# Kernel optimization log

Measured on AMD Instinct MI355X. Metric: run time of the kernel, lower is better.

Reference implementation:

```python
import jax, jax.numpy as jnp
import numpy as np

N_GRAPHS = 100
BN_EPS = 1e-5
L = 4


def batch_norm(x, gamma, beta):
    # torch BatchNorm1d in training mode: biased batch statistics over the node dim
    mu = jnp.mean(x, axis=0)
    var = jnp.var(x, axis=0)
    return gamma * (x - mu) * jax.lax.rsqrt(var + BN_EPS) + beta


def setup_inputs() -> dict:
    key = jax.random.key(0)
    ks = jax.random.split(key, 24)
    N, E, IN, H, C = 50000, 600000, 128, 128, 10
    s = 0.05
    inp = {
        "h": jax.random.normal(ks[0], (N, IN), jnp.float32),
        "snorm_n": jax.random.uniform(ks[1], (N, 1), jnp.float32),
        "edge_src": jax.random.randint(ks[2], (E,), 0, N, jnp.int32),
        "edge_dst": jax.random.randint(ks[3], (E,), 0, N, jnp.int32),
        "graph_ids": jnp.sort(jax.random.randint(ks[4], (N,), 0, N_GRAPHS, jnp.int32)),
        # embedding_h
        "emb_W": jax.random.normal(ks[5], (IN, H), jnp.float32) * s,
        "emb_b": jnp.zeros((H,), jnp.float32),
        # per-layer GIN params, stacked over L layers
        "eps": jnp.zeros((L,), jnp.float32),
        "W1": jax.random.normal(ks[6], (L, H, H), jnp.float32) * s,
        "b1": jnp.zeros((L, H), jnp.float32),
        "g1": jnp.ones((L, H), jnp.float32),   # MLP internal BN gamma
        "be1": jnp.zeros((L, H), jnp.float32),  # MLP internal BN beta
        "W2": jax.random.normal(ks[7], (L, H, H), jnp.float32) * s,
        "b2": jnp.zeros((L, H), jnp.float32),
        "ga": jnp.ones((L, H), jnp.float32),    # ApplyNodeFunc BN gamma
        "ba": jnp.zeros((L, H), jnp.float32),
        "gl": jnp.ones((L, H), jnp.float32),    # GINLayer node BN gamma
        "bl": jnp.zeros((L, H), jnp.float32),
        # linears_prediction (L+1 of them)
        "pred_W": jax.random.normal(ks[8], (L + 1, H, C), jnp.float32) * s,
        "pred_b": jnp.zeros((L + 1, C), jnp.float32),
    }
    return inp


def reference(h, snorm_n, edge_src, edge_dst, graph_ids, emb_W, emb_b, eps,
              W1, b1, g1, be1, W2, b2, ga, ba, gl, bl, pred_W, pred_b):
    N = h.shape[0]
    h = h @ emb_W + emb_b  # embedding_h
    hidden_rep = [h]
    for i in range(L):
        h_in = h
        # sum-aggregate neighbor features (irregular gather + scatter-add)
        neigh = jax.ops.segment_sum(h[edge_src], edge_dst, num_segments=N)
        z = (1.0 + eps[i]) * h + neigh
        # ApplyNodeFunc: MLP (lin->BN->relu->lin) then BN then relu
        z = jax.nn.relu(batch_norm(z @ W1[i] + b1[i], g1[i], be1[i]))
        z = z @ W2[i] + b2[i]
        z = jax.nn.relu(batch_norm(z, ga[i], ba[i]))
        z = z * snorm_n                      # graph_norm
        z = batch_norm(z, gl[i], bl[i])      # batch_norm
        z = jax.nn.relu(z)
        h = h_in + z                         # residual (dropout p=0)
        hidden_rep.append(h)
    score = jnp.zeros((N_GRAPHS, pred_W.shape[-1]), h.dtype)
    for i, hr in enumerate(hidden_rep):
        pooled = jax.ops.segment_sum(hr, graph_ids, num_segments=N_GRAPHS)
        score = score + pooled @ pred_W[i] + pred_b[i]
    return score
```

## Files before the change

kernel.cpp:

```cpp
#include <hip/hip_runtime.h>

#define HD __device__ __forceinline__

static constexpr int H = 128;
static constexpr int G = 100;
static constexpr int L = 4;
static constexpr int C = 10;
static constexpr int DEGCAP = 64;

typedef __attribute__((ext_vector_type(8))) short short8;
typedef __attribute__((ext_vector_type(4))) float f32x4;

HD float bf2f(unsigned int u16) {
    return __uint_as_float(u16 << 16);
}
HD unsigned int f2bf(float f) {
    unsigned int u = __float_as_uint(f);
    u += 0x7fffu + ((u >> 16) & 1u);
    return u >> 16;
}

__global__ __launch_bounds__(256) void prep_kernel(
    const float* __restrict__ embW, const float* __restrict__ W1, const float* __restrict__ W2,
    unsigned short* __restrict__ WT, unsigned short* __restrict__ Hb,
    const int* __restrict__ src, const int* __restrict__ dst, int E,
    int* __restrict__ cnt, int* __restrict__ esrc) {
    int b = blockIdx.x;
    if (b < 576) {
        int mat = b >> 6;
        int bx = b & 63;
        if (b == 0 && threadIdx.x < 64)
            ((unsigned int*)Hb)[threadIdx.x] = 0u;
        const float* s = (mat == 0) ? embW
                       : (mat <= L) ? W1 + (size_t)(mat - 1) * H * H
                                    : W2 + (size_t)(mat - 1 - L) * H * H;
        int t = bx * 256 + threadIdx.x;
        int col = t >> 7, k = t & 127;
        WT[(size_t)mat * H * H + col * H + k] = (unsigned short)f2bf(s[(size_t)k * H + col]);
    } else {
        int e = (b - 576) * 256 + threadIdx.x;
        if (e < E) {
            int d = dst[e];
            int pos = atomicAdd(&cnt[d], 1) & (DEGCAP - 1);
            esrc[(size_t)d * DEGCAP + pos] = src[e] + 1;
        }
    }
}

__global__ __launch_bounds__(256) void agg_kernel(const unsigned short* __restrict__ HbZ,
                                                  const int* __restrict__ cnt,
                                                  const int* __restrict__ esrc,
                                                  const float* __restrict__ eps, int layer,
                                                  unsigned short* __restrict__ ZB, int N) {
    int node = blockIdx.x * 4 + (threadIdx.x >> 6);
    int lane = threadIdx.x & 63;
    if (node >= N) return;
    const unsigned int* H2 = (const unsigned int*)HbZ;
    float e1 = 1.0f + eps[layer];
    unsigned int hv = H2[(size_t)(node + 1) * 64 + lane];
    float ax = e1 * bf2f(hv & 0xffffu);
    float ay = e1 * bf2f(hv >> 16);
    int deg = min(cnt[node], DEGCAP);
    int degPad = min((deg + 15) & ~15, DEGCAP);
    const int* ep = esrc + (size_t)node * DEGCAP;
    for (int j = 0; j < degPad; j += 16) {
        unsigned int v[16];
#pragma unroll
        for (int u = 0; u < 16; ++u) v[u] = H2[(size_t)ep[j + u] * 64 + lane];
        float sx[4] = {0.f, 0.f, 0.f, 0.f}, sy[4] = {0.f, 0.f, 0.f, 0.f};
#pragma unroll
        for (int u = 0; u < 16; ++u) {
            sx[u & 3] += bf2f(v[u] & 0xffffu);
            sy[u & 3] += bf2f(v[u] >> 16);
        }
        ax += (sx[0] + sx[1]) + (sx[2] + sx[3]);
        ay += (sy[0] + sy[1]) + (sy[2] + sy[3]);
    }
    ((unsigned int*)ZB)[(size_t)node * 64 + lane] = f2bf(ax) | (f2bf(ay) << 16);
}

template <bool ABF16, bool TRANS, bool STATS, bool POOLF, bool HOFF>
__global__ __launch_bounds__(256, 4) void mgemm_kernel(
    const float* __restrict__ Af, const unsigned short* __restrict__ Ab,
    const unsigned short* __restrict__ WT, const float* __restrict__ bias,
    const float* __restrict__ sum_in, const float* __restrict__ sq_in,
    const float* __restrict__ gam, const float* __restrict__ bet, float invN,
    unsigned short* __restrict__ outB,
    int N, float* __restrict__ sum_out, float* __restrict__ sq_out,
    const int* __restrict__ gids, float* __restrict__ pool) {
    __shared__ unsigned short As[64 * 136];
    __shared__ float cas[H], ccs[H];
    int tid = threadIdx.x;
    int w = tid >> 6, lane = tid & 63, q = lane >> 4, m = lane & 15;
    int row0 = blockIdx.x * 64;
    int colbase = w * 32;

    short8 bfrag[2][4];
#pragma unroll
    for (int nt = 0; nt < 2; ++nt) {
        const unsigned short* wc = WT + (size_t)(colbase + nt * 16 + m) * H;
#pragma unroll
        for (int kk = 0; kk < 4; ++kk)
            bfrag[nt][kk] = *(const short8*)&wc[kk * 32 + q * 8];
    }

    if (TRANS) {
        if (tid < H) {
            float mu = sum_in[tid] * invN;
            float var = sq_in[tid] * invN - mu * mu;
            float inv = rsqrtf(var + 1e-5f);
            float a = gam[tid] * inv;
            cas[tid] = a;
            ccs[tid] = bet[tid] - mu * a;
        }
        __syncthreads();
    }

    {
        int cc = tid & 15, rg = tid >> 4;
        int c0 = cc * 8;
        float a8[8], b8[8];
        if (TRANS) {
#pragma unroll
            for (int j = 0; j < 8; ++j) { a8[j] = cas[c0 + j]; b8[j] = ccs[c0 + j]; }
        }
#pragma unroll
        for (int rr = 0; rr < 4; ++rr) {
            int r = rg * 4 + rr;
            int gr = row0 + r;
            uint4 o = {0u, 0u, 0u, 0u};
            if (ABF16 && !TRANS) {
                if (gr < N) o = *(const uint4*)&Ab[(size_t)gr * H + c0];
            } else {
                float v[8] = {0.f, 0.f, 0.f, 0.f, 0.f, 0.f, 0.f, 0.f};
                if (gr < N) {
                    if (ABF16) {
                        uint4 x = *(const uint4*)&Ab[(size_t)gr * H + c0];
                        v[0] = bf2f(x.x & 0xffffu); v[1] = bf2f(x.x >> 16);
                        v[2] = bf2f(x.y & 0xffffu); v[3] = bf2f(x.y >> 16);
                        v[4] = bf2f(x.z & 0xffffu); v[5] = bf2f(x.z >> 16);
                        v[6] = bf2f(x.w & 0xffffu); v[7] = bf2f(x.w >> 16);
                    } else {
                        float4 x0 = *(const float4*)&Af[(size_t)gr * H + c0];
                        float4 x1 = *(const float4*)&Af[(size_t)gr * H + c0 + 4];
                        v[0] = x0.x; v[1] = x0.y; v[2] = x0.z; v[3] = x0.w;
                        v[4] = x1.x; v[5] = x1.y; v[6] = x1.z; v[7] = x1.w;
                    }
                }
                if (TRANS) {
#pragma unroll
                    for (int j = 0; j < 8; ++j) v[j] = fmaxf(a8[j] * v[j] + b8[j], 0.f);
                }
                o.x = f2bf(v[0]) | (f2bf(v[1]) << 16);
                o.y = f2bf(v[2]) | (f2bf(v[3]) << 16);
                o.z = f2bf(v[4]) | (f2bf(v[5]) << 16);
                o.w = f2bf(v[6]) | (f2bf(v[7]) << 16);
            }
            *(uint4*)&As[r * 136 + c0] = o;
        }
    }
    __syncthreads();

    f32x4 acc[4][2];
#pragma unroll
    for (int mt = 0; mt < 4; ++mt)
#pragma unroll
        for (int nt = 0; nt < 2; ++nt) acc[mt][nt] = (f32x4){0.f, 0.f, 0.f, 0.f};
#pragma unroll
    for (int kk = 0; kk < 4; ++kk) {
        short8 af[4];
#pragma unroll
        for (int mt = 0; mt < 4; ++mt)
            af[mt] = *(const short8*)&As[(mt * 16 + m) * 136 + kk * 32 + q * 8];
#pragma unroll
        for (int mt = 0; mt < 4; ++mt)
#pragma unroll
            for (int nt = 0; nt < 2; ++nt)
                acc[mt][nt] = __builtin_amdgcn_mfma_f32_16x16x32_bf16(
                    af[mt], bfrag[nt][kk], acc[mt][nt], 0, 0, 0);
    }

    float bs2[2] = {bias[colbase + m], bias[colbase + 16 + m]};
    float s[2] = {0.f, 0.f}, qq[2] = {0.f, 0.f};
#pragma unroll
    for (int mt = 0; mt < 4; ++mt)
#pragma unroll
        for (int nt = 0; nt < 2; ++nt) {
            int gcol = colbase + nt * 16 + m;
#pragma unroll
            for (int rg = 0; rg < 4; ++rg) {
                int grow = row0 + mt * 16 + q * 4 + rg;
                float v = acc[mt][nt][rg] + bs2[nt];
                if (grow < N) {
                    outB[(size_t)(HOFF ? grow + 1 : grow) * H + gcol] = (unsigned short)f2bf(v);
                    if (STATS || POOLF) {
                        s[nt] += v;
                        if (STATS) qq[nt] += v * v;
                    }
                }
            }
        }

    if (STATS) {
#pragma unroll
        for (int nt = 0; nt < 2; ++nt) {
            float sv = s[nt], qv = qq[nt];
            sv += __shfl_xor(sv, 16); sv += __shfl_xor(sv, 32);
            qv += __shfl_xor(qv, 16); qv += __shfl_xor(qv, 32);
            if (q == 0) {
                atomicAdd(&sum_out[colbase + nt * 16 + m], sv);
                atomicAdd(&sq_out[colbase + nt * 16 + m], qv);
            }
        }
    }

    if (POOLF) {
        int last = min(row0 + 63, N - 1);
        bool uni = (gids[row0] == gids[last]);
        if (uni) {
            int g = gids[row0];
#pragma unroll
            for (int nt = 0; nt < 2; ++nt) {
                float sv = s[nt];
                sv += __shfl_xor(sv, 16); sv += __shfl_xor(sv, 32);
                if (q == 0) atomicAdd(&pool[g * H + colbase + nt * 16 + m], sv);
            }
        } else {
#pragma unroll
            for (int mt = 0; mt < 4; ++mt)
#pragma unroll
                for (int nt = 0; nt < 2; ++nt)
#pragma unroll
                    for (int rg = 0; rg < 4; ++rg) {
                        int grow = row0 + mt * 16 + q * 4 + rg;
                        if (grow < N) {
                            float v = acc[mt][nt][rg] + bs2[nt];
                            atomicAdd(&pool[gids[grow] * H + colbase + nt * 16 + m], v);
                        }
                    }
        }
    }
}

__global__ __launch_bounds__(256) void statsv_kernel(const unsigned short* __restrict__ UB,
                                                     const float* __restrict__ snorm,
                                                     const float* __restrict__ sum2, const float* __restrict__ sq2,
                                                     const float* __restrict__ ga, const float* __restrict__ ba,
                                                     float invN, int N,
                                                     float* __restrict__ sum3, float* __restrict__ sq3) {
    __shared__ float cas[H], ccs[H];
    int t = threadIdx.x;
    if (t < H) {
        float m = sum2[t] * invN;
        float var = sq2[t] * invN - m * m;
        float inv = rsqrtf(var + 1e-5f);
        float a = ga[t] * inv;
        cas[t] = a;
        ccs[t] = ba[t] - m * a;
    }
    __syncthreads();
    int col2 = t & 63, part = t >> 6;
    int c0 = col2 * 2, c1 = c0 + 1;
    float a0 = cas[c0], b0 = ccs[c0], a1 = cas[c1], b1 = ccs[c1];
    float s0 = 0.f, q0 = 0.f, s1 = 0.f, q1 = 0.f;
    const unsigned int* U2 = (const unsigned int*)UB;
    for (int r = blockIdx.x * 4 + part; r < N; r += gridDim.x * 4) {
        float sn = snorm[r];
        unsigned int v = U2[(size_t)r * 64 + col2];
        float v0 = fmaxf(a0 * bf2f(v & 0xffffu) + b0, 0.f) * sn;
        float v1 = fmaxf(a1 * bf2f(v >> 16) + b1, 0.f) * sn;
        s0 += v0; q0 += v0 * v0;
        s1 += v1; q1 += v1 * v1;
    }
    __shared__ float S[4][H], Q[4][H];
    S[part][c0] = s0; S[part][c1] = s1;
    Q[part][c0] = q0; Q[part][c1] = q1;
    __syncthreads();
    if (t < H) {
        atomicAdd(&sum3[t], S[0][t] + S[1][t] + S[2][t] + S[3][t]);
        atomicAdd(&sq3[t], Q[0][t] + Q[1][t] + Q[2][t] + Q[3][t]);
    }
}

__global__ __launch_bounds__(256) void tail_kernel(unsigned short* __restrict__ HbZ,
                                                   const unsigned short* __restrict__ UB,
                                                   const float* __restrict__ snorm,
                                                   const float* __restrict__ sum2, const float* __restrict__ sq2,
                                                   const float* __restrict__ ga, const float* __restrict__ ba,
                                                   const float* __restrict__ sum3, const float* __restrict__ sq3,
                                                   const float* __restrict__ gl, const float* __restrict__ bl,
                                                   float invN, const int* __restrict__ gids,
                                                   float* __restrict__ pool, int N) {
    __shared__ float ca2[H], cc2[H], ca3[H], cc3[H];
    __shared__ float PS[8][H];
    int t = threadIdx.x;
    if (t < H) {
        float m2 = sum2[t] * invN, v2 = sq2[t] * invN - m2 * m2;
        float i2 = rsqrtf(v2 + 1e-5f), a2 = ga[t] * i2;
        ca2[t] = a2; cc2[t] = ba[t] - m2 * a2;
        float m3 = sum3[t] * invN, v3 = sq3[t] * invN - m3 * m3;
        float i3 = rsqrtf(v3 + 1e-5f), a3 = gl[t] * i3;
        ca3[t] = a3; cc3[t] = bl[t] - m3 * a3;
    }
    __syncthreads();
    int row0 = blockIdx.x * 32;
    int col4 = t & 31, rowg = t >> 5;
    int c0 = col4 * 4;
    float A2[4], B2[4], A3[4], B3[4];
#pragma unroll
    for (int j = 0; j < 4; ++j) {
        A2[j] = ca2[c0 + j]; B2[j] = cc2[c0 + j];
        A3[j] = ca3[c0 + j]; B3[j] = cc3[c0 + j];
    }
    bool uni = (gids[row0] == gids[min(row0 + 31, N - 1)]);
    float p[4] = {0.f, 0.f, 0.f, 0.f};
    const uint2* U4 = (const uint2*)UB;
    uint2* H4 = (uint2*)HbZ;
#pragma unroll
    for (int rr = 0; rr < 4; ++rr) {
        int r = row0 + rowg * 4 + rr;
        if (r < N) {
            float sn = snorm[r];
            uint2 uv = U4[(size_t)r * 32 + col4];
            uint2 hv = H4[(size_t)(r + 1) * 32 + col4];
            float u[4] = {bf2f(uv.x & 0xffffu), bf2f(uv.x >> 16), bf2f(uv.y & 0xffffu), bf2f(uv.y >> 16)};
            float h[4] = {bf2f(hv.x & 0xffffu), bf2f(hv.x >> 16), bf2f(hv.y & 0xffffu), bf2f(hv.y >> 16)};
#pragma unroll
            for (int j = 0; j < 4; ++j) {
                float v = fmaxf(A2[j] * u[j] + B2[j], 0.f) * sn;
                h[j] += fmaxf(A3[j] * v + B3[j], 0.f);
            }
            uint2 hb;
            hb.x = f2bf(h[0]) | (f2bf(h[1]) << 16);
            hb.y = f2bf(h[2]) | (f2bf(h[3]) << 16);
            H4[(size_t)(r + 1) * 32 + col4] = hb;
            if (uni) {
                p[0] += h[0]; p[1] += h[1]; p[2] += h[2]; p[3] += h[3];
            } else {
                int g = gids[r];
#pragma unroll
                for (int j = 0; j < 4; ++j) atomicAdd(&pool[g * H + c0 + j], h[j]);
            }
        }
    }
    if (uni) {
#pragma unroll
        for (int j = 0; j < 4; ++j) PS[rowg][c0 + j] = p[j];
        __syncthreads();
        if (t < H) {
            float s = PS[0][t] + PS[1][t] + PS[2][t] + PS[3][t] +
                      PS[4][t] + PS[5][t] + PS[6][t] + PS[7][t];
            atomicAdd(&pool[gids[row0] * H + t], s);
        }
    }
}

__global__ void final_kernel(const float* __restrict__ pool, const float* __restrict__ pw,
                             const float* __restrict__ pb, float* __restrict__ out) {
    int g = blockIdx.x, t = threadIdx.x;
    __shared__ float p[H];
    float acc = 0.f;
    for (int i = 0; i <= L; ++i) {
        p[t] = pool[(size_t)(i * G + g) * H + t];
        __syncthreads();
        if (t < C) {
            float s = 0.f;
            for (int f = 0; f < H; ++f) s += p[f] * pw[(size_t)(i * H + f) * C + t];
            acc += s + pb[i * C + t];
        }
        __syncthreads();
    }
    if (t < C) out[g * C + t] = acc;
}

extern "C" void kernel_launch(void* const* d_in, const int* in_sizes, int n_in,
                              void* d_out, int out_size, void* d_ws, size_t ws_size,
                              hipStream_t stream) {
    const float* h_in  = (const float*)d_in[0];
    const float* snorm = (const float*)d_in[1];
    const int* esrc_in = (const int*)d_in[2];
    const int* edst_in = (const int*)d_in[3];
    const int* gids    = (const int*)d_in[4];
    const float* embW = (const float*)d_in[5];
    const float* embB = (const float*)d_in[6];
    const float* eps  = (const float*)d_in[7];
    const float* W1   = (const float*)d_in[8];
    const float* b1   = (const float*)d_in[9];
    const float* g1   = (const float*)d_in[10];
    const float* be1  = (const float*)d_in[11];
    const float* W2   = (const float*)d_in[12];
    const float* b2   = (const float*)d_in[13];
    const float* ga   = (const float*)d_in[14];
    const float* ba   = (const float*)d_in[15];
    const float* gl   = (const float*)d_in[16];
    const float* bl   = (const float*)d_in[17];
    const float* predW = (const float*)d_in[18];
    const float* predB = (const float*)d_in[19];

    const int N = in_sizes[0] / H;
    const int E = in_sizes[2];
    const float invN = 1.0f / (float)N;

    float* ws = (float*)d_ws;
    float* POOL = ws;
    float* STATS = POOL + (size_t)(L + 1) * G * H;
    int* CNT = (int*)(STATS + (size_t)L * 6 * H);
    int* ESRC = CNT + N;
    unsigned short* WT = (unsigned short*)(ESRC + (size_t)N * DEGCAP);
    unsigned short* Hb = WT + (size_t)9 * H * H;
    unsigned short* ZB = Hb + (size_t)(N + 1) * H;
    unsigned short* TB = ZB + (size_t)N * H;
    unsigned short* UB = ZB;

    size_t zbytes = ((size_t)(L + 1) * G * H + (size_t)L * 6 * H + N + (size_t)N * DEGCAP) * 4;
    hipMemsetAsync(POOL, 0, zbytes, stream);

    int prep_blocks = 576 + (E + 255) / 256;
    prep_kernel<<<prep_blocks, 256, 0, stream>>>(embW, W1, W2, WT, Hb,
                                                 esrc_in, edst_in, E, CNT, ESRC);

    int gblocks = (N + 63) / 64;
    mgemm_kernel<false, false, false, true, true><<<gblocks, 256, 0, stream>>>(
        h_in, nullptr, WT, embB, nullptr, nullptr, nullptr, nullptr, invN,
        Hb, N, nullptr, nullptr, gids, POOL);

    for (int i = 0; i < L; ++i) {
        float* S1 = STATS + (size_t)i * 6 * H;
        float* Q1 = S1 + H;
        float* S2 = Q1 + H;
        float* Q2 = S2 + H;
        float* S3 = Q2 + H;
        float* Q3 = S3 + H;
        agg_kernel<<<(N + 3) / 4, 256, 0, stream>>>(Hb, CNT, ESRC, eps, i, ZB, N);
        mgemm_kernel<true, false, true, false, false><<<gblocks, 256, 0, stream>>>(
            nullptr, ZB, WT + (size_t)(1 + i) * H * H, b1 + (size_t)i * H,
            nullptr, nullptr, nullptr, nullptr, invN,
            TB, N, S1, Q1, nullptr, nullptr);
        mgemm_kernel<true, true, true, false, false><<<gblocks, 256, 0, stream>>>(
            nullptr, TB, WT + (size_t)(1 + L + i) * H * H, b2 + (size_t)i * H,
            S1, Q1, g1 + (size_t)i * H, be1 + (size_t)i * H, invN,
            UB, N, S2, Q2, nullptr, nullptr);
        statsv_kernel<<<256, 256, 0, stream>>>(UB, snorm, S2, Q2,
                                               ga + (size_t)i * H, ba + (size_t)i * H, invN, N, S3, Q3);
        tail_kernel<<<(N + 31) / 32, 256, 0, stream>>>(Hb, UB, snorm,
                                                       S2, Q2, ga + (size_t)i * H, ba + (size_t)i * H,
                                                       S3, Q3, gl + (size_t)i * H, bl + (size_t)i * H,
                                                       invN, gids, POOL + (size_t)(i + 1) * G * H, N);
    }
    final_kernel<<<G, H, 0, stream>>>(POOL, predW, predB, (float*)d_out);
}
```

Measured before the change: 693.2 us.

## Fuse neighbor aggregation with first MLP GEMM and BN statistics

Result: faster. 673.4 us (-2.9%).

```diff
diff --git a/kernel.cpp b/kernel.cpp
--- a/kernel.cpp
+++ b/kernel.cpp
@@ -47,36 +47,108 @@
     }
 }
 
-__global__ __launch_bounds__(256) void agg_kernel(const unsigned short* __restrict__ HbZ,
-                                                  const int* __restrict__ cnt,
-                                                  const int* __restrict__ esrc,
-                                                  const float* __restrict__ eps, int layer,
-                                                  unsigned short* __restrict__ ZB, int N) {
-    int node = blockIdx.x * 4 + (threadIdx.x >> 6);
-    int lane = threadIdx.x & 63;
-    if (node >= N) return;
-    const unsigned int* H2 = (const unsigned int*)HbZ;
-    float e1 = 1.0f + eps[layer];
-    unsigned int hv = H2[(size_t)(node + 1) * 64 + lane];
-    float ax = e1 * bf2f(hv & 0xffffu);
-    float ay = e1 * bf2f(hv >> 16);
-    int deg = min(cnt[node], DEGCAP);
-    int degPad = min((deg + 15) & ~15, DEGCAP);
-    const int* ep = esrc + (size_t)node * DEGCAP;
-    for (int j = 0; j < degPad; j += 16) {
-        unsigned int v[16];
-#pragma unroll
-        for (int u = 0; u < 16; ++u) v[u] = H2[(size_t)ep[j + u] * 64 + lane];
-        float sx[4] = {0.f, 0.f, 0.f, 0.f}, sy[4] = {0.f, 0.f, 0.f, 0.f};
-#pragma unroll
-        for (int u = 0; u < 16; ++u) {
-            sx[u & 3] += bf2f(v[u] & 0xffffu);
-            sy[u & 3] += bf2f(v[u] >> 16);
-        }
-        ax += (sx[0] + sx[1]) + (sx[2] + sx[3]);
-        ay += (sy[0] + sy[1]) + (sy[2] + sy[3]);
-    }
-    ((unsigned int*)ZB)[(size_t)node * 64 + lane] = f2bf(ax) | (f2bf(ay) << 16);
+__global__ __launch_bounds__(1024, 2) void aggemm_kernel(
+    const unsigned short* __restrict__ HbZ, const int* __restrict__ cnt,
+    const int* __restrict__ esrc, const float* __restrict__ eps, int layer,
+    const unsigned short* __restrict__ WT, const float* __restrict__ bias,
+    unsigned short* __restrict__ outB, int N,
+    float* __restrict__ sum_out, float* __restrict__ sq_out) {
+    __shared__ unsigned short As[64 * 136];
+    int tid = threadIdx.x;
+    int w = tid >> 6, lane = tid & 63, q = lane >> 4, m = lane & 15;
+    int row0 = blockIdx.x * 64;
+
+    {
+        const unsigned int* H2 = (const unsigned int*)HbZ;
+        float e1 = 1.0f + eps[layer];
+#pragma unroll
+        for (int i = 0; i < 4; ++i) {
+            int r = w * 4 + i;
+            int node = row0 + r;
+            unsigned int out = 0;
+            if (node < N) {
+                unsigned int hv = H2[(size_t)(node + 1) * 64 + lane];
+                float ax = e1 * bf2f(hv & 0xffffu);
+                float ay = e1 * bf2f(hv >> 16);
+                int deg = min(cnt[node], DEGCAP);
+                int degPad = min((deg + 15) & ~15, DEGCAP);
+                const int* ep = esrc + (size_t)node * DEGCAP;
+                for (int j = 0; j < degPad; j += 16) {
+                    unsigned int v[16];
+#pragma unroll
+                    for (int u = 0; u < 16; ++u) v[u] = H2[(size_t)ep[j + u] * 64 + lane];
+                    float sx[4] = {0.f, 0.f, 0.f, 0.f}, sy[4] = {0.f, 0.f, 0.f, 0.f};
+#pragma unroll
+                    for (int u = 0; u < 16; ++u) {
+                        sx[u & 3] += bf2f(v[u] & 0xffffu);
+                        sy[u & 3] += bf2f(v[u] >> 16);
+                    }
+                    ax += (sx[0] + sx[1]) + (sx[2] + sx[3]);
+                    ay += (sy[0] + sy[1]) + (sy[2] + sy[3]);
+                }
+                out = f2bf(ax) | (f2bf(ay) << 16);
+            }
+            *(unsigned int*)&As[r * 136 + lane * 2] = out;
+        }
+    }
+    __syncthreads();
+
+    int mrow = (w >> 2) * 16;
+    int colbase = (w & 3) * 32;
+    short8 bfrag[2][4];
+#pragma unroll
+    for (int nt = 0; nt < 2; ++nt) {
+        const unsigned short* wc = WT + (size_t)(colbase + nt * 16 + m) * H;
+#pragma unroll
+        for (int kk = 0; kk < 4; ++kk)
+            bfrag[nt][kk] = *(const short8*)&wc[kk * 32 + q * 8];
+    }
+    f32x4 acc[2] = {(f32x4){0.f, 0.f, 0.f, 0.f}, (f32x4){0.f, 0.f, 0.f, 0.f}};
+#pragma unroll
+    for (int kk = 0; kk < 4; ++kk) {
+        short8 af = *(const short8*)&As[(mrow + m) * 136 + kk * 32 + q * 8];
+#pragma unroll
+        for (int nt = 0; nt < 2; ++nt)
+            acc[nt] = __builtin_amdgcn_mfma_f32_16x16x32_bf16(af, bfrag[nt][kk], acc[nt], 0, 0, 0);
+    }
+
+    float bs2[2] = {bias[colbase + m], bias[colbase + 16 + m]};
+    float s[2] = {0.f, 0.f}, qq[2] = {0.f, 0.f};
+#pragma unroll
+    for (int nt = 0; nt < 2; ++nt) {
+        int gcol = colbase + nt * 16 + m;
+#pragma unroll
+        for (int rg = 0; rg < 4; ++rg) {
+            int grow = row0 + mrow + q * 4 + rg;
+            float v = acc[nt][rg] + bs2[nt];
+            if (grow < N) {
+                outB[(size_t)grow * H + gcol] = (unsigned short)f2bf(v);
+                s[nt] += v;
+                qq[nt] += v * v;
+            }
+        }
+    }
+#pragma unroll
+    for (int nt = 0; nt < 2; ++nt) {
+        s[nt] += __shfl_xor(s[nt], 16); s[nt] += __shfl_xor(s[nt], 32);
+        qq[nt] += __shfl_xor(qq[nt], 16); qq[nt] += __shfl_xor(qq[nt], 32);
+    }
+    __syncthreads();
+    float* SS = (float*)As;
+    float* QQ = SS + 4 * H;
+    if (q == 0) {
+#pragma unroll
+        for (int nt = 0; nt < 2; ++nt) {
+            int col = colbase + nt * 16 + m;
+            SS[(w >> 2) * H + col] = s[nt];
+            QQ[(w >> 2) * H + col] = qq[nt];
+        }
+    }
+    __syncthreads();
+    if (tid < H) {
+        atomicAdd(&sum_out[tid], SS[tid] + SS[H + tid] + SS[2 * H + tid] + SS[3 * H + tid]);
+        atomicAdd(&sq_out[tid], QQ[tid] + QQ[H + tid] + QQ[2 * H + tid] + QQ[3 * H + tid]);
+    }
 }
 
 template <bool ABF16, bool TRANS, bool STATS, bool POOLF, bool HOFF>
@@ -431,11 +503,9 @@
         float* Q2 = S2 + H;
         float* S3 = Q2 + H;
         float* Q3 = S3 + H;
-        agg_kernel<<<(N + 3) / 4, 256, 0, stream>>>(Hb, CNT, ESRC, eps, i, ZB, N);
-        mgemm_kernel<true, false, true, false, false><<<gblocks, 256, 0, stream>>>(
-            nullptr, ZB, WT + (size_t)(1 + i) * H * H, b1 + (size_t)i * H,
-            nullptr, nullptr, nullptr, nullptr, invN,
-            TB, N, S1, Q1, nullptr, nullptr);
+        aggemm_kernel<<<gblocks, 1024, 0, stream>>>(
+            Hb, CNT, ESRC, eps, i, WT + (size_t)(1 + i) * H * H, b1 + (size_t)i * H,
+            TB, N, S1, Q1);
         mgemm_kernel<true, true, true, false, false><<<gblocks, 256, 0, stream>>>(
             nullptr, TB, WT + (size_t)(1 + L + i) * H * H, b2 + (size_t)i * H,
             S1, Q1, g1 + (size_t)i * H, be1 + (size_t)i * H, invN,
```
